# Kernel optimization log

Measured on AMD Instinct MI355X. Metric: run time of the kernel, lower is better.

The kernel has to match this reference:

```python
import jax, jax.numpy as jnp
import numpy as np

EPS = 1e-5

def _conv3x3(x, w, b):
    # x: [B,C,H,W], w: [O,I,3,3], b: [O]; padding=1 preserves HxW
    y = jax.lax.conv_general_dilated(
        x, w, window_strides=(1, 1), padding=((1, 1), (1, 1)),
        dimension_numbers=('NCHW', 'OIHW', 'NCHW'))
    return y + b[None, :, None, None]

def _instance_norm(x):
    # InstanceNorm2d(affine=False): normalize over spatial dims per (sample, channel)
    mu = jnp.mean(x, axis=(2, 3), keepdims=True)
    var = jnp.var(x, axis=(2, 3), keepdims=True)
    return (x - mu) * jax.lax.rsqrt(var + EPS)

def setup_inputs() -> dict:
    key = jax.random.key(0)
    k1, k2, k3 = jax.random.split(key, 3)
    B, Cin, Cout, H, W = 8, 32, 64, 320, 320
    x = jax.random.normal(k1, (B, Cin, H, W), dtype=jnp.float32)
    w1 = jax.random.normal(k2, (Cout, Cin, 3, 3), dtype=jnp.float32) * (1.0 / np.sqrt(Cin * 9))
    b1 = jnp.zeros((Cout,), dtype=jnp.float32)
    w2 = jax.random.normal(k3, (Cout, Cout, 3, 3), dtype=jnp.float32) * (1.0 / np.sqrt(Cout * 9))
    b2 = jnp.zeros((Cout,), dtype=jnp.float32)
    return {"x": x, "w1": w1, "b1": b1, "w2": w2, "b2": b2}

def reference(x, w1, b1, w2, b2):
    # conv1 -> InstanceNorm -> ReLU -> (Dropout p=0 identity)
    h = jax.nn.relu(_instance_norm(_conv3x3(x, w1, b1)))
    # conv2 -> InstanceNorm -> ReLU -> (Dropout p=0 identity)
    out = jax.nn.relu(_instance_norm(_conv3x3(h, w2, b2)))
    return out
```

## Files before the change

kernel.cpp:

```cpp
#include <hip/hip_runtime.h>

#define HH 320
#define WW 320
#define BB 8
static constexpr float EPS = 1e-5f;

typedef __attribute__((ext_vector_type(8))) short bf16x8;
typedef __attribute__((ext_vector_type(4))) float f32x4;

__device__ inline float bf2f(unsigned short u) {
    union { unsigned int i; float f; } v; v.i = ((unsigned int)u) << 16; return v.f;
}
__device__ inline unsigned short f2bf(float f) {
    union { float f; unsigned int i; } v; v.f = f;
    unsigned int r = v.i + 0x7fffu + ((v.i >> 16) & 1u);
    return (unsigned short)(r >> 16);
}
__device__ inline unsigned int cvtpk(float a, float b) {
    unsigned int r;
    asm volatile("v_cvt_pk_bf16_f32 %0, %1, %2" : "=v"(r) : "v"(a), "v"(b));
    return r;
}
__device__ inline void glds16(const void* g, void* l) {
    __builtin_amdgcn_global_load_lds(
        (const __attribute__((address_space(1))) unsigned int*)g,
        (__attribute__((address_space(3))) unsigned int*)l, 16, 0, 0);
}

__global__ __launch_bounds__(256) void prep_hwc(const float* __restrict__ in,
                                                unsigned short* __restrict__ out)
{
    __shared__ float sT[32][65];
    const int tid = threadIdx.x;
    const int x0  = blockIdx.x * 64;
    const int y   = blockIdx.y;
    const int b   = blockIdx.z;
    for (int e = tid; e < 32 * 64; e += 256) {
        int c = e >> 6, x = e & 63;
        sT[c][x] = in[(((size_t)(b * 32 + c) * HH) + y) * WW + x0 + x];
    }
    __syncthreads();
    for (int e = tid; e < 64 * 32; e += 256) {
        int x = e >> 5, c = e & 31;
        out[((((size_t)b * HH + y) * WW) + x0 + x) * 32 + c] = f2bf(sT[c][x]);
    }
}

__global__ __launch_bounds__(256) void wprep_swz(const float* __restrict__ w1,
                                                 const float* __restrict__ w2,
                                                 unsigned short* __restrict__ wt1,
                                                 unsigned short* __restrict__ wt2)
{
    int i = blockIdx.x * 256 + threadIdx.x;
    if (i < 2304) {
        int s = i & 3, oc = (i >> 2) & 63, kk = i >> 8;
        int icq = s ^ ((oc >> 1) & 3);
        const float* src = w1 + ((size_t)oc * 32 + icq * 8) * 9 + kk;
        unsigned short pk[8];
#pragma unroll
        for (int j = 0; j < 8; ++j) pk[j] = f2bf(src[j * 9]);
        *(bf16x8*)&wt1[(size_t)i * 8] = *(bf16x8*)pk;
    }
    if (i < 4608) {
        int icc = i / 2304, u = i - icc * 2304;
        int s = u & 3, oc = (u >> 2) & 63, kk = u >> 8;
        int icq = s ^ ((oc >> 1) & 3);
        const float* src = w2 + ((size_t)oc * 64 + icc * 32 + icq * 8) * 9 + kk;
        unsigned short pk[8];
#pragma unroll
        for (int j = 0; j < 8; ++j) pk[j] = f2bf(src[j * 9]);
        *(bf16x8*)&wt2[(size_t)i * 8] = *(bf16x8*)pk;
    }
}

__global__ __launch_bounds__(256) void fold_stats(const float2* __restrict__ partials,
                                                  const float* __restrict__ b2,
                                                  const unsigned short* __restrict__ wt2,
                                                  float2* __restrict__ stats1,
                                                  unsigned short* __restrict__ wt2b,
                                                  float* __restrict__ bias2b)
{
    __shared__ float2 red[4][64];
    __shared__ float sMu[64], sR[64];
    __shared__ float sBias[256];
    const int b = blockIdx.x, tid = threadIdx.x;
    const int oc = tid & 63, q = tid >> 6;

    float s = 0.f, ss = 0.f;
    for (int i = q; i < 100; i += 4) {
        float2 p = partials[((size_t)b * 100 + i) * 64 + oc];
        s += p.x; ss += p.y;
    }
    red[q][oc] = make_float2(s, ss);
    __syncthreads();
    if (tid < 64) {
        float S = 0.f, SS = 0.f;
#pragma unroll
        for (int k = 0; k < 4; ++k) { S += red[k][tid].x; SS += red[k][tid].y; }
        const float n = (float)(HH * WW);
        float mean = S / n;
        float var  = fmaxf(SS / n - mean * mean, 0.f);
        float rstd = rsqrtf(var + EPS);
        stats1[b * 64 + tid] = make_float2(mean, rstd);
        sMu[tid] = bf2f(f2bf(mean));
        sR[tid]  = rstd;
    }
    __syncthreads();

    float bsum = 0.f;
    for (int cs = q * 2; cs < q * 2 + 2; ++cs) {
        int icc = cs >> 2, sdx = cs & 3;
        int icq = sdx ^ ((oc >> 1) & 3);
        for (int kk = 0; kk < 9; ++kk) {
            size_t u = (size_t)icc * 2304 + kk * 256 + oc * 4 + sdx;
            bf16x8 v = *(const bf16x8*)&wt2[u * 8];
            unsigned short o8[8];
#pragma unroll
            for (int j = 0; j < 8; ++j) {
                int ic = icc * 32 + icq * 8 + j;
                unsigned short wb = f2bf(bf2f(((unsigned short*)&v)[j]) * sR[ic]);
                o8[j] = wb;
                bsum += bf2f(wb) * sMu[ic];
            }
            *(bf16x8*)&wt2b[((size_t)b * 4608 + u) * 8] = *(bf16x8*)o8;
        }
    }
    sBias[tid] = bsum;
    __syncthreads();
    if (tid < 64) {
        float t = sBias[tid] + sBias[tid + 64] + sBias[tid + 128] + sBias[tid + 192];
        bias2b[b * 64 + tid] = b2[tid] - t;
    }
}

__global__ __launch_bounds__(256, 2) void conv1_super(
    const unsigned short* __restrict__ in_hwc,
    const unsigned short* __restrict__ wt,
    const float* __restrict__ bias,
    unsigned short* __restrict__ out_hwc,
    float2* __restrict__ partials)
{
    constexpr int NG = 4;
    constexpr int NS = 12;

    __shared__ __align__(16) unsigned short sA[2][6 * 264 * 8];
    __shared__ __align__(16) unsigned short sWb[2][768 * 8];
    __shared__ float sRedS[256];
    __shared__ float sRedSS[256];

    const int tid = threadIdx.x;
    const int x0  = blockIdx.x * 64;
    const int yb  = blockIdx.y * 16;
    const int b   = blockIdx.z;
    const int w   = tid >> 6;
    const int l   = tid & 63;
    const int lm  = l & 15;
    const int g   = l >> 4;

    auto stage_slab = [&](int s2, int buf) {
        int kt2 = s2 % 3;
        const unsigned short* wsrc = wt + (size_t)(kt2 * 768) * 8;
        unsigned short* dst = &sWb[buf][0];
#pragma unroll
        for (int k = 0; k < 3; ++k)
            glds16(wsrc + (size_t)(k * 256 + w * 64 + l) * 8,
                   dst + (size_t)(k * 256 + w * 64) * 8);
    };

    auto issueA_glds = [&](int gi2) {
        int y02 = yb + gi2 * 4;
        unsigned short* buf = &sA[gi2 & 1][0];
        for (int r = w; r < 6; r += 4) {
            int gy = y02 + r - 1;
            unsigned short* ldsrow = buf + r * 2112;
            if ((unsigned)gy < HH) {
                const unsigned short* rowbase =
                    in_hwc + ((size_t)(b * HH + gy) * WW) * 32;
#pragma unroll
                for (int i = 0; i < 4; ++i) {
                    int u  = 4 + i * 64 + l;
                    int x  = u >> 2;
                    int cs = (u & 3) ^ ((x >> 1) & 3);
                    glds16(rowbase + (size_t)(x0 + x - 1) * 32 + cs * 8,
                           ldsrow + (size_t)(4 + i * 64) * 8);
                }
            } else {
                for (int u2 = l; u2 < 264; u2 += 64)
                    *(bf16x8*)(ldsrow + u2 * 8) = (bf16x8){0,0,0,0,0,0,0,0};
            }
        }
        if (tid < 48) {
            int icq = tid & 3, side = (tid >> 2) & 1, r = tid >> 3;
            int xs = side ? 65 : 0;
            int gy = y02 + r - 1, gx = x0 + xs - 1;
            bf16x8 v = (bf16x8){0,0,0,0,0,0,0,0};
            if ((unsigned)gy < HH && (unsigned)gx < WW)
                v = *(const bf16x8*)&in_hwc[(((size_t)(b * HH + gy) * WW) + gx) * 32 + icq * 8];
            *(bf16x8*)&buf[(r * 264 + xs * 4 + icq) * 8] = v;
        }
    };

    f32x4 acc[4][4];
#pragma unroll
    for (int fp = 0; fp < 4; ++fp)
#pragma unroll
        for (int fo = 0; fo < 4; ++fo)
            acc[fp][fo] = (f32x4){0.f, 0.f, 0.f, 0.f};

    float bb[4][4];
#pragma unroll
    for (int fo = 0; fo < 4; ++fo) {
        float4 b4 = *(const float4*)&bias[fo * 16 + g * 4];
        bb[fo][0] = b4.x; bb[fo][1] = b4.y; bb[fo][2] = b4.z; bb[fo][3] = b4.w;
    }
    float sjA[4][4] = {}, qjA[4][4] = {};

    stage_slab(0, 0);
    issueA_glds(0);
    __syncthreads();

    for (int s = 0; s < NS; ++s) {
        const int kt = s % 3;
        const int gi = s / 3;

        if (s + 1 < NS) stage_slab(s + 1, (s + 1) & 1);
        if (kt == 0 && gi + 1 < NG) issueA_glds(gi + 1);

        {
            const unsigned short* bufA = &sA[gi & 1][0];
            const unsigned short* bufW = &sWb[s & 1][0];
            __builtin_amdgcn_s_setprio(1);
#pragma unroll
            for (int kx = 0; kx < 3; ++kx) {
                bf16x8 af[4], bfr[4];
#pragma unroll
                for (int fp = 0; fp < 4; ++fp) {
                    int xl = fp * 16 + lm + kx;
                    int u  = (xl * 4 + g) ^ ((xl >> 1) & 3);
                    af[fp] = *(const bf16x8*)(bufA + ((w + kt) * 264 + u) * 8);
                }
#pragma unroll
                for (int fo = 0; fo < 4; ++fo) {
                    int ocr = fo * 16 + lm;
                    int p   = (kx * 64 + ocr) * 4 + (g ^ ((ocr >> 1) & 3));
                    bfr[fo] = *(const bf16x8*)(bufW + p * 8);
                }
#pragma unroll
                for (int fo = 0; fo < 4; ++fo)
#pragma unroll
                    for (int fp = 0; fp < 4; ++fp)
                        acc[fp][fo] = __builtin_amdgcn_mfma_f32_16x16x32_bf16(
                            bfr[fo], af[fp], acc[fp][fo], 0, 0, 0);
            }
            __builtin_amdgcn_s_setprio(0);
        }

        if (kt == 2) {
            const int row = yb + 4 * gi + w;
#pragma unroll
            for (int fo = 0; fo < 4; ++fo) {
#pragma unroll
                for (int fp = 0; fp < 4; ++fp) {
                    float v0 = acc[fp][fo][0] + bb[fo][0], v1 = acc[fp][fo][1] + bb[fo][1];
                    float v2 = acc[fp][fo][2] + bb[fo][2], v3 = acc[fp][fo][3] + bb[fo][3];
                    sjA[fo][0] += v0; qjA[fo][0] += v0 * v0;
                    sjA[fo][1] += v1; qjA[fo][1] += v1 * v1;
                    sjA[fo][2] += v2; qjA[fo][2] += v2 * v2;
                    sjA[fo][3] += v3; qjA[fo][3] += v3 * v3;
                    uint2 st = make_uint2(cvtpk(v0, v1), cvtpk(v2, v3));
                    *(uint2*)&out_hwc[(((size_t)b * HH + row) * WW + x0 + fp * 16 + lm) * 64 + fo * 16 + g * 4] = st;
                    acc[fp][fo] = (f32x4){0.f, 0.f, 0.f, 0.f};
                }
            }
        }
        __syncthreads();
    }

#pragma unroll
    for (int fo = 0; fo < 4; ++fo) {
#pragma unroll
        for (int m = 1; m <= 8; m <<= 1)
#pragma unroll
            for (int j = 0; j < 4; ++j) {
                sjA[fo][j] += __shfl_xor(sjA[fo][j], m);
                qjA[fo][j] += __shfl_xor(qjA[fo][j], m);
            }
        if (lm == 0) {
#pragma unroll
            for (int j = 0; j < 4; ++j) {
                sRedS [w * 64 + fo * 16 + g * 4 + j] = sjA[fo][j];
                sRedSS[w * 64 + fo * 16 + g * 4 + j] = qjA[fo][j];
            }
        }
    }
    __syncthreads();
    if (tid < 64) {
        float S = 0.f, SS = 0.f;
#pragma unroll
        for (int q = 0; q < 4; ++q) { S += sRedS[q * 64 + tid]; SS += sRedSS[q * 64 + tid]; }
        partials[((size_t)b * 100 + blockIdx.y * 5 + blockIdx.x) * 64 + tid] = make_float2(S, SS);
    }
}

__global__ __launch_bounds__(256, 3) void conv2_tile(
    const unsigned short* __restrict__ in_hwc,
    const float2* __restrict__ stats_in,
    const unsigned short* __restrict__ wt,
    const float* __restrict__ bias,
    unsigned short* __restrict__ out_hwc,
    float2* __restrict__ partials)
{
    __shared__ __align__(16) char smem[38912];
    unsigned short* sA    = (unsigned short*)smem;
    unsigned short* sW    = (unsigned short*)(smem + 25344);
    float*          sMaxMu= (float*)(smem + 37632);
    unsigned short* sMuBf = (unsigned short*)(smem + 37888);
    float* sRedS  = (float*)smem;
    float* sRedSS = (float*)(smem + 1024);

    const int tid = threadIdx.x;
    const int x0  = blockIdx.x * 64;
    const int y0  = blockIdx.y * 4;
    const int b   = blockIdx.z;
    const int w   = tid >> 6;
    const int l   = tid & 63;
    const int lm  = l & 15;
    const int g   = l >> 4;

    const unsigned short* wtb = wt + (size_t)b * 4608 * 8;
    const float* biasb        = bias + b * 64;

    if (tid < 64) {
        float2 ms = stats_in[b * 64 + tid];
        unsigned short mb = f2bf(ms.x);
        sMuBf[tid]  = mb;
        sMaxMu[tid] = bf2f(mb);
    }

    f32x4 acc[4][4];
#pragma unroll
    for (int fp = 0; fp < 4; ++fp)
#pragma unroll
        for (int fo = 0; fo < 4; ++fo)
            acc[fp][fo] = (f32x4){0.f, 0.f, 0.f, 0.f};

    for (int icc = 0; icc < 2; ++icc) {
        __syncthreads();

#pragma unroll
        for (int k = 0; k < 7; ++k) {
            int e = tid + k * 256;
            if (e < 1584) {
                int r = e / 264, rem = e - r * 264;
                int x = rem >> 2, icq = rem & 3;
                int gy = y0 + r - 1, gx = x0 + x - 1;
                int c0 = icc * 32 + icq * 8;
                unsigned int w4[4];
                if ((unsigned)gy < HH && (unsigned)gx < WW) {
                    bf16x8 v = *(const bf16x8*)&in_hwc[(((size_t)(b * HH + gy) * WW) + gx) * 64 + c0];
#pragma unroll
                    for (int jp = 0; jp < 4; ++jp) {
                        float f0 = fmaxf(bf2f(((unsigned short*)&v)[2 * jp]),     sMaxMu[c0 + 2 * jp]);
                        float f1 = fmaxf(bf2f(((unsigned short*)&v)[2 * jp + 1]), sMaxMu[c0 + 2 * jp + 1]);
                        w4[jp] = cvtpk(f0, f1);
                    }
                } else {
#pragma unroll
                    for (int jp = 0; jp < 4; ++jp)
                        w4[jp] = (unsigned int)sMuBf[c0 + 2 * jp] |
                                 ((unsigned int)sMuBf[c0 + 2 * jp + 1] << 16);
                }
                *(uint4*)&sA[(r * 264 + x * 4 + (icq ^ ((x >> 1) & 3))) * 8] =
                    make_uint4(w4[0], w4[1], w4[2], w4[3]);
            }
        }

#pragma unroll
        for (int kt = 0; kt < 3; ++kt) {
            if (kt > 0) __syncthreads();
            {
                const unsigned short* wsrc = wtb + ((size_t)icc * 2304 + kt * 768) * 8;
#pragma unroll
                for (int k = 0; k < 3; ++k)
                    glds16(wsrc + (size_t)(k * 256 + w * 64 + l) * 8,
                           sW + (size_t)(k * 256 + w * 64) * 8);
            }
            __syncthreads();

            __builtin_amdgcn_s_setprio(1);
#pragma unroll
            for (int kx = 0; kx < 3; ++kx) {
                bf16x8 af[4], bfr[4];
#pragma unroll
                for (int fp = 0; fp < 4; ++fp) {
                    int xl = fp * 16 + lm + kx;
                    int u  = (xl * 4 + g) ^ ((xl >> 1) & 3);
                    af[fp] = *(const bf16x8*)&sA[((w + kt) * 264 + u) * 8];
                }
#pragma unroll
                for (int fo = 0; fo < 4; ++fo) {
                    int ocr = fo * 16 + lm;
                    int p   = (kx * 256 + ocr * 4 + (g ^ ((ocr >> 1) & 3)));
                    bfr[fo] = *(const bf16x8*)&sW[p * 8];
                }
#pragma unroll
                for (int fo = 0; fo < 4; ++fo)
#pragma unroll
                    for (int fp = 0; fp < 4; ++fp)
                        acc[fp][fo] = __builtin_amdgcn_mfma_f32_16x16x32_bf16(
                            bfr[fo], af[fp], acc[fp][fo], 0, 0, 0);
            }
            __builtin_amdgcn_s_setprio(0);
        }
    }

    __syncthreads();

    const int row = y0 + w;
#pragma unroll
    for (int fo = 0; fo < 4; ++fo) {
        float4 b4 = *(const float4*)&biasb[fo * 16 + g * 4];
        float bb[4] = {b4.x, b4.y, b4.z, b4.w};
        float sj[4] = {0,0,0,0}, qj[4] = {0,0,0,0};
#pragma unroll
        for (int fp = 0; fp < 4; ++fp) {
            float v0 = acc[fp][fo][0] + bb[0], v1 = acc[fp][fo][1] + bb[1];
            float v2 = acc[fp][fo][2] + bb[2], v3 = acc[fp][fo][3] + bb[3];
            sj[0] += v0; qj[0] += v0 * v0;  sj[1] += v1; qj[1] += v1 * v1;
            sj[2] += v2; qj[2] += v2 * v2;  sj[3] += v3; qj[3] += v3 * v3;
            uint2 st = make_uint2(cvtpk(v0, v1), cvtpk(v2, v3));
            *(uint2*)&out_hwc[(((size_t)b * HH + row) * WW + x0 + fp * 16 + lm) * 64 + fo * 16 + g * 4] = st;
        }
#pragma unroll
        for (int m = 1; m <= 8; m <<= 1)
#pragma unroll
            for (int j = 0; j < 4; ++j) {
                sj[j] += __shfl_xor(sj[j], m);
                qj[j] += __shfl_xor(qj[j], m);
            }
        if (lm == 0) {
#pragma unroll
            for (int j = 0; j < 4; ++j) {
                sRedS [w * 64 + fo * 16 + g * 4 + j] = sj[j];
                sRedSS[w * 64 + fo * 16 + g * 4 + j] = qj[j];
            }
        }
    }
    __syncthreads();
    if (tid < 64) {
        float S = 0.f, SS = 0.f;
#pragma unroll
        for (int q = 0; q < 4; ++q) { S += sRedS[q * 64 + tid]; SS += sRedSS[q * 64 + tid]; }
        partials[((size_t)b * 400 + blockIdx.y * 5 + blockIdx.x) * 64 + tid] = make_float2(S, SS);
    }
}

__global__ __launch_bounds__(256) void reduce_stats(const float2* __restrict__ partials,
                                                    float2* __restrict__ stats, int count)
{
    const int b  = blockIdx.x;
    const int oc = threadIdx.x & 63;
    const int q  = threadIdx.x >> 6;
    float s = 0.f, ss = 0.f;
    for (int i = q; i < count; i += 4) {
        float2 p = partials[((size_t)b * count + i) * 64 + oc];
        s += p.x; ss += p.y;
    }
    __shared__ float2 red[4][64];
    red[q][oc] = make_float2(s, ss);
    __syncthreads();
    if (threadIdx.x < 64) {
        float S = 0.f, SS = 0.f;
#pragma unroll
        for (int k = 0; k < 4; ++k) { S += red[k][threadIdx.x].x; SS += red[k][threadIdx.x].y; }
        const float n = (float)(HH * WW);
        float mean = S / n;
        float var  = fmaxf(SS / n - mean * mean, 0.f);
        stats[b * 64 + threadIdx.x] = make_float2(mean, rsqrtf(var + EPS));
    }
}

__global__ __launch_bounds__(256) void finalize_t(const unsigned short* __restrict__ h2,
                                                  const float2* __restrict__ stats,
                                                  float* __restrict__ out)
{
    __shared__ float2 sSt[64];
    const int tid = threadIdx.x;
    const int b   = blockIdx.z;
    if (tid < 64) sSt[tid] = stats[b * 64 + tid];
    __syncthreads();
    const int r   = tid >> 6;
    const int px  = tid & 63;
    const int row = blockIdx.y * 4 + r;
    const int x   = blockIdx.x * 64 + px;
    const unsigned short* src = h2 + ((size_t)(b * HH + row) * WW + x) * 64;
    bf16x8 v[8];
#pragma unroll
    for (int cq = 0; cq < 8; ++cq) v[cq] = *(const bf16x8*)(src + cq * 8);
#pragma unroll
    for (int cq = 0; cq < 8; ++cq)
#pragma unroll
        for (int j = 0; j < 8; ++j) {
            int c = cq * 8 + j;
            float2 ms = sSt[c];
            float f = fmaxf((bf2f(((unsigned short*)&v[cq])[j]) - ms.x) * ms.y, 0.f);
            out[((size_t)(b * 64 + c) * HH + row) * WW + x] = f;
        }
}

extern "C" void kernel_launch(void* const* d_in, const int* in_sizes, int n_in,
                              void* d_out, int out_size, void* d_ws, size_t ws_size,
                              hipStream_t stream)
{
    const float* x  = (const float*)d_in[0];
    const float* w1 = (const float*)d_in[1];
    const float* b1 = (const float*)d_in[2];
    const float* w2 = (const float*)d_in[3];
    const float* b2 = (const float*)d_in[4];
    float* out = (float*)d_out;

    char* ws = (char*)d_ws;
    unsigned short* h    = (unsigned short*)ws;
    float2* partials     = (float2*)(ws + 104857600);
    float2* stats1       = (float2*)(ws + 104857600 + 1638400);
    float2* stats2       = (float2*)(ws + 104857600 + 1638400 + 4096);
    unsigned short* reg2 = (unsigned short*)(ws + 104857600 + 1638400 + 8192);
    unsigned short* x_hwc = reg2;
    unsigned short* h2    = reg2;

    char* ob = (char*)d_out + 209715200;
    float*          bias2b = (float*)(ob - 2048);
    unsigned short* wt2b   = (unsigned short*)(ob - 2048 - 589824);
    unsigned short* wt2    = (unsigned short*)(ob - 2048 - 589824 - 73728);
    unsigned short* wt1    = (unsigned short*)(ob - 2048 - 589824 - 73728 - 36864);

    wprep_swz<<<18, 256, 0, stream>>>(w1, w2, wt1, wt2);
    prep_hwc<<<dim3(5, HH, BB), 256, 0, stream>>>(x, x_hwc);

    conv1_super<<<dim3(5, 20, BB), 256, 0, stream>>>(x_hwc, wt1, b1, h, partials);
    fold_stats<<<BB, 256, 0, stream>>>(partials, b2, wt2, stats1, wt2b, bias2b);
    conv2_tile<<<dim3(5, 80, BB), 256, 0, stream>>>(h, stats1, wt2b, bias2b, h2, partials);
    reduce_stats<<<BB, 256, 0, stream>>>(partials, stats2, 400);
    finalize_t<<<dim3(5, 80, BB), 256, 0, stream>>>(h2, stats2, out);
}
```

Before: 334.4 us.

## Fuse NCHW fp32 to HWC bf16 input conversion into conv1 tile loader

Drops the separate prep_hwc transpose kernel. conv1 now reads the fp32 NCHW input directly, converts it to bf16 with packed conversion and writes it into the swizzled LDS tile layout. This removes a full write and re-read of the bf16 HWC copy of the input, plus one kernel launch. In exchange the loader uses synchronous strided scalar global loads instead of asynchronous global-to-LDS copies, which may reduce overlap with the MFMA compute.

Result: slower. 365.9 us (+9.4%).

```diff
diff --git a/kernel.cpp b/kernel.cpp
--- a/kernel.cpp
+++ b/kernel.cpp
@@ -25,25 +25,6 @@
     __builtin_amdgcn_global_load_lds(
         (const __attribute__((address_space(1))) unsigned int*)g,
         (__attribute__((address_space(3))) unsigned int*)l, 16, 0, 0);
-}
-
-__global__ __launch_bounds__(256) void prep_hwc(const float* __restrict__ in,
-                                                unsigned short* __restrict__ out)
-{
-    __shared__ float sT[32][65];
-    const int tid = threadIdx.x;
-    const int x0  = blockIdx.x * 64;
-    const int y   = blockIdx.y;
-    const int b   = blockIdx.z;
-    for (int e = tid; e < 32 * 64; e += 256) {
-        int c = e >> 6, x = e & 63;
-        sT[c][x] = in[(((size_t)(b * 32 + c) * HH) + y) * WW + x0 + x];
-    }
-    __syncthreads();
-    for (int e = tid; e < 64 * 32; e += 256) {
-        int x = e >> 5, c = e & 31;
-        out[((((size_t)b * HH + y) * WW) + x0 + x) * 32 + c] = f2bf(sT[c][x]);
-    }
 }
 
 __global__ __launch_bounds__(256) void wprep_swz(const float* __restrict__ w1,
@@ -133,8 +114,8 @@
     }
 }
 
-__global__ __launch_bounds__(256, 2) void conv1_super(
-    const unsigned short* __restrict__ in_hwc,
+__global__ __launch_bounds__(256, 2) void conv1_fused(
+    const float* __restrict__ xin,
     const unsigned short* __restrict__ wt,
     const float* __restrict__ bias,
     unsigned short* __restrict__ out_hwc,
@@ -167,36 +148,31 @@
                    dst + (size_t)(k * 256 + w * 64) * 8);
     };
 
-    auto issueA_glds = [&](int gi2) {
-        int y02 = yb + gi2 * 4;
+    auto issueA_f32 = [&](int gi2) {
+        const int y02 = yb + gi2 * 4;
         unsigned short* buf = &sA[gi2 & 1][0];
-        for (int r = w; r < 6; r += 4) {
-            int gy = y02 + r - 1;
-            unsigned short* ldsrow = buf + r * 2112;
-            if ((unsigned)gy < HH) {
-                const unsigned short* rowbase =
-                    in_hwc + ((size_t)(b * HH + gy) * WW) * 32;
-#pragma unroll
-                for (int i = 0; i < 4; ++i) {
-                    int u  = 4 + i * 64 + l;
-                    int x  = u >> 2;
-                    int cs = (u & 3) ^ ((x >> 1) & 3);
-                    glds16(rowbase + (size_t)(x0 + x - 1) * 32 + cs * 8,
-                           ldsrow + (size_t)(4 + i * 64) * 8);
-                }
-            } else {
-                for (int u2 = l; u2 < 264; u2 += 64)
-                    *(bf16x8*)(ldsrow + u2 * 8) = (bf16x8){0,0,0,0,0,0,0,0};
-            }
-        }
-        if (tid < 48) {
-            int icq = tid & 3, side = (tid >> 2) & 1, r = tid >> 3;
-            int xs = side ? 65 : 0;
-            int gy = y02 + r - 1, gx = x0 + xs - 1;
-            bf16x8 v = (bf16x8){0,0,0,0,0,0,0,0};
-            if ((unsigned)gy < HH && (unsigned)gx < WW)
-                v = *(const bf16x8*)&in_hwc[(((size_t)(b * HH + gy) * WW) + gx) * 32 + icq * 8];
-            *(bf16x8*)&buf[(r * 264 + xs * 4 + icq) * 8] = v;
+#pragma unroll
+        for (int k = 0; k < 13; ++k) {
+            int e = tid + k * 256;
+            if (e < 3168) {
+                int cq  = e / 396;
+                int rem = e - cq * 396;
+                int r   = rem / 66;
+                int x   = rem - r * 66;
+                int gy  = y02 + r - 1, gx = x0 + x - 1;
+                float v0 = 0.f, v1 = 0.f, v2 = 0.f, v3 = 0.f;
+                if ((unsigned)gy < HH && (unsigned)gx < WW) {
+                    const float* src = xin + (((size_t)(b * 32 + cq * 4) * HH) + gy) * WW + gx;
+                    v0 = src[0];
+                    v1 = src[(size_t)HH * WW];
+                    v2 = src[(size_t)2 * HH * WW];
+                    v3 = src[(size_t)3 * HH * WW];
+                }
+                uint2 pk = make_uint2(cvtpk(v0, v1), cvtpk(v2, v3));
+                int icq  = cq >> 1, half = cq & 1;
+                int u    = x * 4 + (icq ^ ((x >> 1) & 3));
+                *(uint2*)&buf[(r * 264 + u) * 8 + half * 4] = pk;
+            }
         }
     };
 
@@ -216,7 +192,7 @@
     float sjA[4][4] = {}, qjA[4][4] = {};
 
     stage_slab(0, 0);
-    issueA_glds(0);
+    issueA_f32(0);
     __syncthreads();
 
     for (int s = 0; s < NS; ++s) {
@@ -224,7 +200,7 @@
         const int gi = s / 3;
 
         if (s + 1 < NS) stage_slab(s + 1, (s + 1) & 1);
-        if (kt == 0 && gi + 1 < NG) issueA_glds(gi + 1);
+        if (kt == 0 && gi + 1 < NG) issueA_f32(gi + 1);
 
         {
             const unsigned short* bufA = &sA[gi & 1][0];
@@ -524,9 +500,7 @@
     float2* partials     = (float2*)(ws + 104857600);
     float2* stats1       = (float2*)(ws + 104857600 + 1638400);
     float2* stats2       = (float2*)(ws + 104857600 + 1638400 + 4096);
-    unsigned short* reg2 = (unsigned short*)(ws + 104857600 + 1638400 + 8192);
-    unsigned short* x_hwc = reg2;
-    unsigned short* h2    = reg2;
+    unsigned short* h2   = (unsigned short*)(ws + 104857600 + 1638400 + 8192);
 
     char* ob = (char*)d_out + 209715200;
     float*          bias2b = (float*)(ob - 2048);
@@ -535,9 +509,8 @@
     unsigned short* wt1    = (unsigned short*)(ob - 2048 - 589824 - 73728 - 36864);
 
     wprep_swz<<<18, 256, 0, stream>>>(w1, w2, wt1, wt2);
-    prep_hwc<<<dim3(5, HH, BB), 256, 0, stream>>>(x, x_hwc);
-
-    conv1_super<<<dim3(5, 20, BB), 256, 0, stream>>>(x_hwc, wt1, b1, h, partials);
+
+    conv1_fused<<<dim3(5, 20, BB), 256, 0, stream>>>(x, wt1, b1, h, partials);
     fold_stats<<<BB, 256, 0, stream>>>(partials, b2, wt2, stats1, wt2b, bias2b);
     conv2_tile<<<dim3(5, 80, BB), 256, 0, stream>>>(h, stats1, wt2b, bias2b, h2, partials);
     reduce_stats<<<BB, 256, 0, stream>>>(partials, stats2, 400);
```
